# Kernel tuning notes

Hardware: AMD Instinct MI355X
Metric: run time of the kernel (lower is better)

The kernel has to match this reference:

```python
import jax, jax.numpy as jnp
import numpy as np

N, K, C = 10000, 64, 128


def setup_inputs() -> dict:
    key = jax.random.key(0)
    ks = jax.random.split(key, 6)
    return {
        "real": jax.random.normal(ks[0], (N, C), dtype=jnp.float32),
        "imag": jax.random.normal(ks[1], (N, C), dtype=jnp.float32),
        "Qreal": jax.random.normal(ks[2], (N, K), dtype=jnp.float32) / np.sqrt(N),
        "Qimag": jax.random.normal(ks[3], (N, K), dtype=jnp.float32) / np.sqrt(N),
        "Ritz": jax.random.uniform(ks[4], (K,), dtype=jnp.float32),
        "weight": jax.random.normal(ks[5], (C, C), dtype=jnp.float32) * np.sqrt(2.0 / (C + C)),  # xavier-ish scale
        "long_diff": 5,
    }


def reference(real, imag, Qreal, Qimag, Ritz, weight, long_diff):
    # TT = Ritz ** long_diff ; spectral filters L = Q diag(TT) Q^H split into real/imag
    TT = jnp.power(Ritz, long_diff)  # [K]
    QrT = Qreal * TT  # [N,K] columns scaled by TT (== Qreal @ diag(TT))
    QiT = Qimag * TT
    L_real = QrT @ Qreal.T + QiT @ Qimag.T  # [N,N]
    L_imag = QiT @ Qreal.T - QrT @ Qimag.T  # [N,N]
    # complex spmm + shared dense weight: (L @ X_complex) @ W
    res_real = (L_real @ real - L_imag @ imag) @ weight  # [N,C]
    res_imag = (L_imag @ real + L_real @ imag) @ weight  # [N,C]
    # complex ReLU: mask by sign of real part
    mask = (res_real >= 0).astype(res_real.dtype)
    return real + mask * res_real, imag + mask * res_imag
```

## Files before the change

kernel.cpp:

```cpp
#include <hip/hip_runtime.h>

#define NN 10000
#define KK 64
#define CC 128
#define OUTOFF (NN * CC)

__device__ __forceinline__ float4 f4fma(float s, float4 v, float4 a) {
    a.x += s * v.x; a.y += s * v.y; a.z += s * v.z; a.w += s * v.w;
    return a;
}

__global__ __launch_bounds__(512) void kA(const float* __restrict__ re,
                                          const float* __restrict__ im,
                                          const float* __restrict__ Qr,
                                          const float* __restrict__ Qi,
                                          float* __restrict__ part, int nA)
{
    __shared__ float4 sQr[16][16];
    __shared__ float4 sQi[16][16];
    __shared__ float4 sRe[16][32];
    __shared__ float4 sIm[16][32];

    const int t  = threadIdx.x;
    const int kt = t & 15;
    const int ct = t >> 4;

    float aU[4][4], aV[4][4];
#pragma unroll
    for (int a = 0; a < 4; ++a)
#pragma unroll
        for (int b = 0; b < 4; ++b) { aU[a][b] = 0.f; aV[a][b] = 0.f; }

    for (int cb = blockIdx.x; cb < 625; cb += nA) {
        const int n0 = cb * 16;
        for (int i = t; i < 1536; i += 512) {
            if (i < 256) {
                int row = i >> 4, q = i & 15;
                sQr[row][q] = ((const float4*)(Qr + (size_t)(n0 + row) * KK))[q];
            } else if (i < 512) {
                int j = i - 256, row = j >> 4, q = j & 15;
                sQi[row][q] = ((const float4*)(Qi + (size_t)(n0 + row) * KK))[q];
            } else if (i < 1024) {
                int j = i - 512, row = j >> 5, q = j & 31;
                sRe[row][q] = ((const float4*)(re + (size_t)(n0 + row) * CC))[q];
            } else {
                int j = i - 1024, row = j >> 5, q = j & 31;
                sIm[row][q] = ((const float4*)(im + (size_t)(n0 + row) * CC))[q];
            }
        }
        __syncthreads();
#pragma unroll 4
        for (int r = 0; r < 16; ++r) {
            float4 q_r = sQr[r][kt];
            float4 q_i = sQi[r][kt];
            float4 x_r = sRe[r][ct];
            float4 x_i = sIm[r][ct];
            float qr[4] = {q_r.x, q_r.y, q_r.z, q_r.w};
            float qi[4] = {q_i.x, q_i.y, q_i.z, q_i.w};
            float xr[4] = {x_r.x, x_r.y, x_r.z, x_r.w};
            float xi[4] = {x_i.x, x_i.y, x_i.z, x_i.w};
#pragma unroll
            for (int a = 0; a < 4; ++a)
#pragma unroll
                for (int b = 0; b < 4; ++b) {
                    aU[a][b] += qr[a] * xr[b] + qi[a] * xi[b];
                    aV[a][b] += qi[a] * xr[b] - qr[a] * xi[b];
                }
        }
        __syncthreads();
    }
    float* base = part + (size_t)blockIdx.x * 16384;
    const int k0 = kt * 4, c0 = ct * 4;
#pragma unroll
    for (int a = 0; a < 4; ++a) {
        *(float4*)(base + (k0 + a) * CC + c0)        = make_float4(aU[a][0], aU[a][1], aU[a][2], aU[a][3]);
        *(float4*)(base + 8192 + (k0 + a) * CC + c0) = make_float4(aV[a][0], aV[a][1], aV[a][2], aV[a][3]);
    }
}

__global__ __launch_bounds__(256) void kR(const float* __restrict__ part,
                                          float* __restrict__ UV, int nA)
{
    __shared__ float red[256];
    const int t  = threadIdx.x;
    const int e0 = blockIdx.x * 32;
    const int ei = t & 31, sl = t >> 5;
    float s = 0.f;
    for (int b = sl; b < nA; b += 8)
        s += part[(size_t)b * 16384 + e0 + ei];
    red[t] = s;
    __syncthreads();
    if (t < 32) {
        float tot = 0.f;
#pragma unroll
        for (int q = 0; q < 8; ++q) tot += red[q * 32 + t];
        UV[e0 + t] = tot;
    }
}

__global__ __launch_bounds__(256) void kB(const float* __restrict__ UV,
                                          const float* __restrict__ Ritz,
                                          const int* __restrict__ ldp,
                                          const float* __restrict__ W,
                                          float* __restrict__ UVW)
{
    __shared__ float rowU[128], rowV[128];
    const int k = blockIdx.x, t = threadIdx.x;
    if (t < 128) rowU[t] = UV[k * 128 + t];
    else         rowV[t - 128] = UV[8192 + k * 128 + (t - 128)];
    __syncthreads();
    const int m = t >> 7, c = t & 127;
    const float* row = m ? rowV : rowU;
    float acc = 0.f;
#pragma unroll 8
    for (int cp = 0; cp < 128; ++cp)
        acc += row[cp] * W[cp * 128 + c];
    const int ld = *ldp;
    const float rz = Ritz[k];
    float tt = 1.f;
    for (int i = 0; i < ld; ++i) tt *= rz;
    UVW[m * 8192 + k * 128 + c] = tt * acc;
}

__global__ __launch_bounds__(256) void kC(const float* __restrict__ re,
                                          const float* __restrict__ im,
                                          const float* __restrict__ Qr,
                                          const float* __restrict__ Qi,
                                          const float* __restrict__ UVW,
                                          float* __restrict__ out)
{
    __shared__ float4 sUW[64][32];
    __shared__ float4 sVW[64][32];
    const int t = threadIdx.x;
    {
        const float4* g = (const float4*)UVW;
        float4* s0 = &sUW[0][0];
        float4* s1 = &sVW[0][0];
        for (int i = t; i < 2048; i += 256) s0[i] = g[i];
        for (int i = t; i < 2048; i += 256) s1[i] = g[2048 + i];
    }
    __syncthreads();
    const int ct = t & 15;
    const int rp = t >> 4;

    for (int cb = blockIdx.x; cb < 313; cb += 256) {
        const int na = cb * 32 + rp * 2;
        if (na >= NN) continue;
        const int nb = na + 1;
        const float4* qra = (const float4*)(Qr + (size_t)na * KK);
        const float4* qia = (const float4*)(Qi + (size_t)na * KK);
        const float4* qrb = (const float4*)(Qr + (size_t)nb * KK);
        const float4* qib = (const float4*)(Qi + (size_t)nb * KK);

        float4 z = make_float4(0.f, 0.f, 0.f, 0.f);
        float4 aR0a = z, aR1a = z, aI0a = z, aI1a = z;
        float4 aR0b = z, aR1b = z, aI0b = z, aI1b = z;

#pragma unroll 4
        for (int k4 = 0; k4 < 16; ++k4) {
            float4 QRa = qra[k4], QIa = qia[k4];
            float4 QRb = qrb[k4], QIb = qib[k4];
            float ar[4] = {QRa.x, QRa.y, QRa.z, QRa.w};
            float ai[4] = {QIa.x, QIa.y, QIa.z, QIa.w};
            float br[4] = {QRb.x, QRb.y, QRb.z, QRb.w};
            float bi[4] = {QIb.x, QIb.y, QIb.z, QIb.w};
#pragma unroll
            for (int j = 0; j < 4; ++j) {
                const int k = k4 * 4 + j;
                float4 uw0 = sUW[k][ct], uw1 = sUW[k][16 + ct];
                float4 vw0 = sVW[k][ct], vw1 = sVW[k][16 + ct];
                aR0a = f4fma(ar[j], uw0, aR0a); aR0a = f4fma(ai[j], vw0, aR0a);
                aR1a = f4fma(ar[j], uw1, aR1a); aR1a = f4fma(ai[j], vw1, aR1a);
                aI0a = f4fma(ai[j], uw0, aI0a); aI0a = f4fma(-ar[j], vw0, aI0a);
                aI1a = f4fma(ai[j], uw1, aI1a); aI1a = f4fma(-ar[j], vw1, aI1a);
                aR0b = f4fma(br[j], uw0, aR0b); aR0b = f4fma(bi[j], vw0, aR0b);
                aR1b = f4fma(br[j], uw1, aR1b); aR1b = f4fma(bi[j], vw1, aR1b);
                aI0b = f4fma(bi[j], uw0, aI0b); aI0b = f4fma(-br[j], vw0, aI0b);
                aI1b = f4fma(bi[j], uw1, aI1b); aI1b = f4fma(-br[j], vw1, aI1b);
            }
        }
        const int c0 = ct * 4;
#pragma unroll
        for (int half = 0; half < 2; ++half) {
            const int cc = c0 + half * 64;
            const float4 aRa = half ? aR1a : aR0a;
            const float4 aIa = half ? aI1a : aI0a;
            const float4 aRb = half ? aR1b : aR0b;
            const float4 aIb = half ? aI1b : aI0b;

            float4 rin = *(const float4*)(re + (size_t)na * CC + cc);
            float4 iin = *(const float4*)(im + (size_t)na * CC + cc);
            float4 orr, oii;
            orr.x = rin.x + (aRa.x >= 0.f ? aRa.x : 0.f); oii.x = iin.x + (aRa.x >= 0.f ? aIa.x : 0.f);
            orr.y = rin.y + (aRa.y >= 0.f ? aRa.y : 0.f); oii.y = iin.y + (aRa.y >= 0.f ? aIa.y : 0.f);
            orr.z = rin.z + (aRa.z >= 0.f ? aRa.z : 0.f); oii.z = iin.z + (aRa.z >= 0.f ? aIa.z : 0.f);
            orr.w = rin.w + (aRa.w >= 0.f ? aRa.w : 0.f); oii.w = iin.w + (aRa.w >= 0.f ? aIa.w : 0.f);
            *(float4*)(out + (size_t)na * CC + cc)          = orr;
            *(float4*)(out + OUTOFF + (size_t)na * CC + cc) = oii;

            rin = *(const float4*)(re + (size_t)nb * CC + cc);
            iin = *(const float4*)(im + (size_t)nb * CC + cc);
            orr.x = rin.x + (aRb.x >= 0.f ? aRb.x : 0.f); oii.x = iin.x + (aRb.x >= 0.f ? aIb.x : 0.f);
            orr.y = rin.y + (aRb.y >= 0.f ? aRb.y : 0.f); oii.y = iin.y + (aRb.y >= 0.f ? aIb.y : 0.f);
            orr.z = rin.z + (aRb.z >= 0.f ? aRb.z : 0.f); oii.z = iin.z + (aRb.z >= 0.f ? aIb.z : 0.f);
            orr.w = rin.w + (aRb.w >= 0.f ? aRb.w : 0.f); oii.w = iin.w + (aRb.w >= 0.f ? aIb.w : 0.f);
            *(float4*)(out + (size_t)nb * CC + cc)          = orr;
            *(float4*)(out + OUTOFF + (size_t)nb * CC + cc) = oii;
        }
    }
}

extern "C" void kernel_launch(void* const* d_in, const int* in_sizes, int n_in,
                              void* d_out, int out_size, void* d_ws, size_t ws_size,
                              hipStream_t stream) {
    const float* re   = (const float*)d_in[0];
    const float* im   = (const float*)d_in[1];
    const float* Qr   = (const float*)d_in[2];
    const float* Qi   = (const float*)d_in[3];
    const float* Ritz = (const float*)d_in[4];
    const float* W    = (const float*)d_in[5];
    const int*   ldp  = (const int*)d_in[6];
    float* out = (float*)d_out;
    float* ws  = (float*)d_ws;

    long avail = ((long)ws_size - 131072L) / 65536L;
    int nA = (int)(avail < 1 ? 1 : (avail > 256 ? 256 : avail));

    float* part = ws;
    float* UV   = ws + (size_t)nA * 16384;
    float* UVW  = UV + 16384;

    kA<<<nA, 512, 0, stream>>>(re, im, Qr, Qi, part, nA);
    kR<<<512, 256, 0, stream>>>(part, UV, nA);
    kB<<<64, 256, 0, stream>>>(UV, Ritz, ldp, W, UVW);
    kC<<<256, 256, 0, stream>>>(re, im, Qr, Qi, UVW, out);
}
```

Measured before the change: 126.7 us.

## Fuse four kernels into one cooperative kernel with grid syncs

Replaces the four separate launches (partial projection, reduction, weight multiply, output expansion) with a single cooperative kernel of 256 blocks of 512 threads, using grid.sync between phases. The first phase also prefetches the next chunk into registers while computing on the current one, and the output phase now gives each thread one row instead of two. The aim is to remove launch gaps and inter-kernel drain. In exchange it adds grid-wide barrier costs and fixes the partial count at 256 regardless of workspace size, and phase 3 runs on only 64 blocks while the rest wait.

```diff
diff --git a/kernel.cpp b/kernel.cpp
--- a/kernel.cpp
+++ b/kernel.cpp
@@ -1,211 +1,187 @@
 #include <hip/hip_runtime.h>
+#include <hip/hip_cooperative_groups.h>
+
+namespace cg = cooperative_groups;
 
 #define NN 10000
 #define KK 64
 #define CC 128
 #define OUTOFF (NN * CC)
+#define NA 256
+#define CHUNKS_A 625
+#define CHUNKS_C 313
 
 __device__ __forceinline__ float4 f4fma(float s, float4 v, float4 a) {
-    a.x += s * v.x; a.y += s * v.y; a.z += s * v.z; a.w += s * v.w;
+    a.x = fmaf(s, v.x, a.x); a.y = fmaf(s, v.y, a.y);
+    a.z = fmaf(s, v.z, a.z); a.w = fmaf(s, v.w, a.w);
     return a;
 }
 
-__global__ __launch_bounds__(512) void kA(const float* __restrict__ re,
-                                          const float* __restrict__ im,
-                                          const float* __restrict__ Qr,
-                                          const float* __restrict__ Qi,
-                                          float* __restrict__ part, int nA)
+__global__ __launch_bounds__(512, 1) void fused(
+    const float* __restrict__ re, const float* __restrict__ im,
+    const float* __restrict__ Qr, const float* __restrict__ Qi,
+    const float* __restrict__ Ritz, const int* __restrict__ ldp,
+    const float* __restrict__ W, float* __restrict__ ws,
+    float* __restrict__ out)
 {
-    __shared__ float4 sQr[16][16];
-    __shared__ float4 sQi[16][16];
-    __shared__ float4 sRe[16][32];
-    __shared__ float4 sIm[16][32];
-
-    const int t  = threadIdx.x;
-    const int kt = t & 15;
-    const int ct = t >> 4;
-
-    float aU[4][4], aV[4][4];
-#pragma unroll
-    for (int a = 0; a < 4; ++a)
-#pragma unroll
-        for (int b = 0; b < 4; ++b) { aU[a][b] = 0.f; aV[a][b] = 0.f; }
-
-    for (int cb = blockIdx.x; cb < 625; cb += nA) {
-        const int n0 = cb * 16;
-        for (int i = t; i < 1536; i += 512) {
-            if (i < 256) {
-                int row = i >> 4, q = i & 15;
-                sQr[row][q] = ((const float4*)(Qr + (size_t)(n0 + row) * KK))[q];
-            } else if (i < 512) {
-                int j = i - 256, row = j >> 4, q = j & 15;
-                sQi[row][q] = ((const float4*)(Qi + (size_t)(n0 + row) * KK))[q];
-            } else if (i < 1024) {
-                int j = i - 512, row = j >> 5, q = j & 31;
-                sRe[row][q] = ((const float4*)(re + (size_t)(n0 + row) * CC))[q];
-            } else {
-                int j = i - 1024, row = j >> 5, q = j & 31;
-                sIm[row][q] = ((const float4*)(im + (size_t)(n0 + row) * CC))[q];
-            }
-        }
-        __syncthreads();
+    __shared__ float4 smem[4096];
+    cg::grid_group grid = cg::this_grid();
+    const int t = threadIdx.x;
+    const int bid = blockIdx.x;
+
+    {
+        const int kt = t & 15;
+        const int ctA = t >> 4;
+        const int row_q = (t & 255) >> 4, q_q = t & 15;
+        const int row_x = t >> 5,          q_x = t & 31;
+        const float4* gq  = (const float4*)((t < 256) ? Qr : Qi);
+        const float4* gre = (const float4*)re;
+        const float4* gim = (const float4*)im;
+
+        float aU[4][4] = {}, aV[4][4] = {};
+
+        int cb = bid;
+        int n0 = cb * 16;
+        float4 r0 = gq [(size_t)(n0 + row_q) * 16 + q_q];
+        float4 r1 = gre[(size_t)(n0 + row_x) * 32 + q_x];
+        float4 r2 = gim[(size_t)(n0 + row_x) * 32 + q_x];
+
+        while (true) {
+            smem[t] = r0; smem[512 + t] = r1; smem[1024 + t] = r2;
+            __syncthreads();
+            const int nx = cb + NA;
+            if (nx < CHUNKS_A) {
+                const int m0 = nx * 16;
+                r0 = gq [(size_t)(m0 + row_q) * 16 + q_q];
+                r1 = gre[(size_t)(m0 + row_x) * 32 + q_x];
+                r2 = gim[(size_t)(m0 + row_x) * 32 + q_x];
+            }
 #pragma unroll 4
-        for (int r = 0; r < 16; ++r) {
-            float4 q_r = sQr[r][kt];
-            float4 q_i = sQi[r][kt];
-            float4 x_r = sRe[r][ct];
-            float4 x_i = sIm[r][ct];
-            float qr[4] = {q_r.x, q_r.y, q_r.z, q_r.w};
-            float qi[4] = {q_i.x, q_i.y, q_i.z, q_i.w};
-            float xr[4] = {x_r.x, x_r.y, x_r.z, x_r.w};
-            float xi[4] = {x_i.x, x_i.y, x_i.z, x_i.w};
-#pragma unroll
-            for (int a = 0; a < 4; ++a)
-#pragma unroll
-                for (int b = 0; b < 4; ++b) {
-                    aU[a][b] += qr[a] * xr[b] + qi[a] * xi[b];
-                    aV[a][b] += qi[a] * xr[b] - qr[a] * xi[b];
+            for (int rr = 0; rr < 16; ++rr) {
+                float4 q_r = smem[rr * 16 + kt];
+                float4 q_i = smem[256 + rr * 16 + kt];
+                float4 x_r = smem[512 + rr * 32 + ctA];
+                float4 x_i = smem[1024 + rr * 32 + ctA];
+                float qr_[4] = {q_r.x, q_r.y, q_r.z, q_r.w};
+                float qi_[4] = {q_i.x, q_i.y, q_i.z, q_i.w};
+                float xr_[4] = {x_r.x, x_r.y, x_r.z, x_r.w};
+                float xi_[4] = {x_i.x, x_i.y, x_i.z, x_i.w};
+#pragma unroll
+                for (int a = 0; a < 4; ++a)
+#pragma unroll
+                    for (int b = 0; b < 4; ++b) {
+                        aU[a][b] = fmaf(qr_[a], xr_[b], aU[a][b]);
+                        aU[a][b] = fmaf(qi_[a], xi_[b], aU[a][b]);
+                        aV[a][b] = fmaf(qi_[a], xr_[b], aV[a][b]);
+                        aV[a][b] = fmaf(-qr_[a], xi_[b], aV[a][b]);
+                    }
+            }
+            __syncthreads();
+            if (nx >= CHUNKS_A) break;
+            cb = nx;
+        }
+        float* base = ws + (size_t)bid * 16384;
+        const int k0 = kt * 4, c0 = ctA * 4;
+#pragma unroll
+        for (int a = 0; a < 4; ++a) {
+            *(float4*)(base + (k0 + a) * CC + c0)        = make_float4(aU[a][0], aU[a][1], aU[a][2], aU[a][3]);
+            *(float4*)(base + 8192 + (k0 + a) * CC + c0) = make_float4(aV[a][0], aV[a][1], aV[a][2], aV[a][3]);
+        }
+    }
+    __threadfence();
+    grid.sync();
+
+    {
+        const int ei = t & 63, sl = t >> 6;
+        float s = 0.f;
+        const float* p = ws + (size_t)sl * 16384 + bid * 64 + ei;
+        for (int b = sl; b < NA; b += 8) { s += *p; p += (size_t)8 * 16384; }
+        float* sf = (float*)smem;
+        sf[t] = s;
+        __syncthreads();
+        if (t < 64) {
+            float tot = 0.f;
+#pragma unroll
+            for (int q = 0; q < 8; ++q) tot += sf[q * 64 + t];
+            ws[(size_t)NA * 16384 + bid * 64 + t] = tot;
+        }
+        __syncthreads();
+    }
+    __threadfence();
+    grid.sync();
+
+    if (bid < KK) {
+        const float* UV = ws + (size_t)NA * 16384;
+        float* sf = (float*)smem;
+        if (t < 256) sf[t] = (t < 128) ? UV[bid * 128 + t]
+                                       : UV[8192 + bid * 128 + (t - 128)];
+        __syncthreads();
+        if (t < 256) {
+            const int m = t >> 7, c = t & 127;
+            const float* rowm = sf + m * 128;
+            float acc = 0.f;
+#pragma unroll 8
+            for (int cp = 0; cp < 128; ++cp)
+                acc = fmaf(rowm[cp], W[cp * 128 + c], acc);
+            const int ld = *ldp;
+            const float rz = Ritz[bid];
+            float tt = 1.f;
+            for (int i = 0; i < ld; ++i) tt *= rz;
+            ws[(size_t)NA * 16384 + 16384 + m * 8192 + bid * 128 + c] = tt * acc;
+        }
+        __syncthreads();
+    }
+    __threadfence();
+    grid.sync();
+
+    {
+        const float4* gUVW = (const float4*)(ws + (size_t)NA * 16384 + 16384);
+        for (int i = t; i < 4096; i += 512) smem[i] = gUVW[i];
+        __syncthreads();
+        const int ct = t & 15;
+        const int r  = t >> 4;
+
+        for (int cb = bid; cb < CHUNKS_C; cb += NA) {
+            const int na = cb * 32 + r;
+            if (na >= NN) continue;
+            const float4* qr4 = (const float4*)(Qr + (size_t)na * KK);
+            const float4* qi4 = (const float4*)(Qi + (size_t)na * KK);
+            float4 z = make_float4(0.f, 0.f, 0.f, 0.f);
+            float4 aR0 = z, aR1 = z, aI0 = z, aI1 = z;
+#pragma unroll 4
+            for (int k4 = 0; k4 < 16; ++k4) {
+                float4 QR = qr4[k4], QI = qi4[k4];
+                float ar[4] = {QR.x, QR.y, QR.z, QR.w};
+                float ai[4] = {QI.x, QI.y, QI.z, QI.w};
+#pragma unroll
+                for (int j = 0; j < 4; ++j) {
+                    const int k = k4 * 4 + j;
+                    float4 uw0 = smem[k * 32 + ct];
+                    float4 uw1 = smem[k * 32 + 16 + ct];
+                    float4 vw0 = smem[2048 + k * 32 + ct];
+                    float4 vw1 = smem[2048 + k * 32 + 16 + ct];
+                    aR0 = f4fma(ar[j], uw0, aR0); aR0 = f4fma(ai[j], vw0, aR0);
+                    aR1 = f4fma(ar[j], uw1, aR1); aR1 = f4fma(ai[j], vw1, aR1);
+                    aI0 = f4fma(ai[j], uw0, aI0); aI0 = f4fma(-ar[j], vw0, aI0);
+                    aI1 = f4fma(ai[j], uw1, aI1); aI1 = f4fma(-ar[j], vw1, aI1);
                 }
-        }
-        __syncthreads();
-    }
-    float* base = part + (size_t)blockIdx.x * 16384;
-    const int k0 = kt * 4, c0 = ct * 4;
-#pragma unroll
-    for (int a = 0; a < 4; ++a) {
-        *(float4*)(base + (k0 + a) * CC + c0)        = make_float4(aU[a][0], aU[a][1], aU[a][2], aU[a][3]);
-        *(float4*)(base + 8192 + (k0 + a) * CC + c0) = make_float4(aV[a][0], aV[a][1], aV[a][2], aV[a][3]);
-    }
-}
-
-__global__ __launch_bounds__(256) void kR(const float* __restrict__ part,
-                                          float* __restrict__ UV, int nA)
-{
-    __shared__ float red[256];
-    const int t  = threadIdx.x;
-    const int e0 = blockIdx.x * 32;
-    const int ei = t & 31, sl = t >> 5;
-    float s = 0.f;
-    for (int b = sl; b < nA; b += 8)
-        s += part[(size_t)b * 16384 + e0 + ei];
-    red[t] = s;
-    __syncthreads();
-    if (t < 32) {
-        float tot = 0.f;
-#pragma unroll
-        for (int q = 0; q < 8; ++q) tot += red[q * 32 + t];
-        UV[e0 + t] = tot;
-    }
-}
-
-__global__ __launch_bounds__(256) void kB(const float* __restrict__ UV,
-                                          const float* __restrict__ Ritz,
-                                          const int* __restrict__ ldp,
-                                          const float* __restrict__ W,
-                                          float* __restrict__ UVW)
-{
-    __shared__ float rowU[128], rowV[128];
-    const int k = blockIdx.x, t = threadIdx.x;
-    if (t < 128) rowU[t] = UV[k * 128 + t];
-    else         rowV[t - 128] = UV[8192 + k * 128 + (t - 128)];
-    __syncthreads();
-    const int m = t >> 7, c = t & 127;
-    const float* row = m ? rowV : rowU;
-    float acc = 0.f;
-#pragma unroll 8
-    for (int cp = 0; cp < 128; ++cp)
-        acc += row[cp] * W[cp * 128 + c];
-    const int ld = *ldp;
-    const float rz = Ritz[k];
-    float tt = 1.f;
-    for (int i = 0; i < ld; ++i) tt *= rz;
-    UVW[m * 8192 + k * 128 + c] = tt * acc;
-}
-
-__global__ __launch_bounds__(256) void kC(const float* __restrict__ re,
-                                          const float* __restrict__ im,
-                                          const float* __restrict__ Qr,
-                                          const float* __restrict__ Qi,
-                                          const float* __restrict__ UVW,
-                                          float* __restrict__ out)
-{
-    __shared__ float4 sUW[64][32];
-    __shared__ float4 sVW[64][32];
-    const int t = threadIdx.x;
-    {
-        const float4* g = (const float4*)UVW;
-        float4* s0 = &sUW[0][0];
-        float4* s1 = &sVW[0][0];
-        for (int i = t; i < 2048; i += 256) s0[i] = g[i];
-        for (int i = t; i < 2048; i += 256) s1[i] = g[2048 + i];
-    }
-    __syncthreads();
-    const int ct = t & 15;
-    const int rp = t >> 4;
-
-    for (int cb = blockIdx.x; cb < 313; cb += 256) {
-        const int na = cb * 32 + rp * 2;
-        if (na >= NN) continue;
-        const int nb = na + 1;
-        const float4* qra = (const float4*)(Qr + (size_t)na * KK);
-        const float4* qia = (const float4*)(Qi + (size_t)na * KK);
-        const float4* qrb = (const float4*)(Qr + (size_t)nb * KK);
-        const float4* qib = (const float4*)(Qi + (size_t)nb * KK);
-
-        float4 z = make_float4(0.f, 0.f, 0.f, 0.f);
-        float4 aR0a = z, aR1a = z, aI0a = z, aI1a = z;
-        float4 aR0b = z, aR1b = z, aI0b = z, aI1b = z;
-
-#pragma unroll 4
-        for (int k4 = 0; k4 < 16; ++k4) {
-            float4 QRa = qra[k4], QIa = qia[k4];
-            float4 QRb = qrb[k4], QIb = qib[k4];
-            float ar[4] = {QRa.x, QRa.y, QRa.z, QRa.w};
-            float ai[4] = {QIa.x, QIa.y, QIa.z, QIa.w};
-            float br[4] = {QRb.x, QRb.y, QRb.z, QRb.w};
-            float bi[4] = {QIb.x, QIb.y, QIb.z, QIb.w};
-#pragma unroll
-            for (int j = 0; j < 4; ++j) {
-                const int k = k4 * 4 + j;
-                float4 uw0 = sUW[k][ct], uw1 = sUW[k][16 + ct];
-                float4 vw0 = sVW[k][ct], vw1 = sVW[k][16 + ct];
-                aR0a = f4fma(ar[j], uw0, aR0a); aR0a = f4fma(ai[j], vw0, aR0a);
-                aR1a = f4fma(ar[j], uw1, aR1a); aR1a = f4fma(ai[j], vw1, aR1a);
-                aI0a = f4fma(ai[j], uw0, aI0a); aI0a = f4fma(-ar[j], vw0, aI0a);
-                aI1a = f4fma(ai[j], uw1, aI1a); aI1a = f4fma(-ar[j], vw1, aI1a);
-                aR0b = f4fma(br[j], uw0, aR0b); aR0b = f4fma(bi[j], vw0, aR0b);
-                aR1b = f4fma(br[j], uw1, aR1b); aR1b = f4fma(bi[j], vw1, aR1b);
-                aI0b = f4fma(bi[j], uw0, aI0b); aI0b = f4fma(-br[j], vw0, aI0b);
-                aI1b = f4fma(bi[j], uw1, aI1b); aI1b = f4fma(-br[j], vw1, aI1b);
-            }
-        }
-        const int c0 = ct * 4;
-#pragma unroll
-        for (int half = 0; half < 2; ++half) {
-            const int cc = c0 + half * 64;
-            const float4 aRa = half ? aR1a : aR0a;
-            const float4 aIa = half ? aI1a : aI0a;
-            const float4 aRb = half ? aR1b : aR0b;
-            const float4 aIb = half ? aI1b : aI0b;
-
-            float4 rin = *(const float4*)(re + (size_t)na * CC + cc);
-            float4 iin = *(const float4*)(im + (size_t)na * CC + cc);
-            float4 orr, oii;
-            orr.x = rin.x + (aRa.x >= 0.f ? aRa.x : 0.f); oii.x = iin.x + (aRa.x >= 0.f ? aIa.x : 0.f);
-            orr.y = rin.y + (aRa.y >= 0.f ? aRa.y : 0.f); oii.y = iin.y + (aRa.y >= 0.f ? aIa.y : 0.f);
-            orr.z = rin.z + (aRa.z >= 0.f ? aRa.z : 0.f); oii.z = iin.z + (aRa.z >= 0.f ? aIa.z : 0.f);
-            orr.w = rin.w + (aRa.w >= 0.f ? aRa.w : 0.f); oii.w = iin.w + (aRa.w >= 0.f ? aIa.w : 0.f);
-            *(float4*)(out + (size_t)na * CC + cc)          = orr;
-            *(float4*)(out + OUTOFF + (size_t)na * CC + cc) = oii;
-
-            rin = *(const float4*)(re + (size_t)nb * CC + cc);
-            iin = *(const float4*)(im + (size_t)nb * CC + cc);
-            orr.x = rin.x + (aRb.x >= 0.f ? aRb.x : 0.f); oii.x = iin.x + (aRb.x >= 0.f ? aIb.x : 0.f);
-            orr.y = rin.y + (aRb.y >= 0.f ? aRb.y : 0.f); oii.y = iin.y + (aRb.y >= 0.f ? aIb.y : 0.f);
-            orr.z = rin.z + (aRb.z >= 0.f ? aRb.z : 0.f); oii.z = iin.z + (aRb.z >= 0.f ? aIb.z : 0.f);
-            orr.w = rin.w + (aRb.w >= 0.f ? aRb.w : 0.f); oii.w = iin.w + (aRb.w >= 0.f ? aIb.w : 0.f);
-            *(float4*)(out + (size_t)nb * CC + cc)          = orr;
-            *(float4*)(out + OUTOFF + (size_t)nb * CC + cc) = oii;
+            }
+            const int c0 = ct * 4;
+#pragma unroll
+            for (int half = 0; half < 2; ++half) {
+                const int cc = c0 + half * 64;
+                const float4 aR = half ? aR1 : aR0;
+                const float4 aI = half ? aI1 : aI0;
+                float4 rin = *(const float4*)(re + (size_t)na * CC + cc);
+                float4 iin = *(const float4*)(im + (size_t)na * CC + cc);
+                float4 orr, oii;
+                orr.x = rin.x + (aR.x >= 0.f ? aR.x : 0.f); oii.x = iin.x + (aR.x >= 0.f ? aI.x : 0.f);
+                orr.y = rin.y + (aR.y >= 0.f ? aR.y : 0.f); oii.y = iin.y + (aR.y >= 0.f ? aI.y : 0.f);
+                orr.z = rin.z + (aR.z >= 0.f ? aR.z : 0.f); oii.z = iin.z + (aR.z >= 0.f ? aI.z : 0.f);
+                orr.w = rin.w + (aR.w >= 0.f ? aR.w : 0.f); oii.w = iin.w + (aR.w >= 0.f ? aI.w : 0.f);
+                *(float4*)(out + (size_t)na * CC + cc)          = orr;
+                *(float4*)(out + OUTOFF + (size_t)na * CC + cc) = oii;
+            }
         }
     }
 }
@@ -223,15 +199,7 @@
     float* out = (float*)d_out;
     float* ws  = (float*)d_ws;
 
-    long avail = ((long)ws_size - 131072L) / 65536L;
-    int nA = (int)(avail < 1 ? 1 : (avail > 256 ? 256 : avail));
-
-    float* part = ws;
-    float* UV   = ws + (size_t)nA * 16384;
-    float* UVW  = UV + 16384;
-
-    kA<<<nA, 512, 0, stream>>>(re, im, Qr, Qi, part, nA);
-    kR<<<512, 256, 0, stream>>>(part, UV, nA);
-    kB<<<64, 256, 0, stream>>>(UV, Ritz, ldp, W, UVW);
-    kC<<<256, 256, 0, stream>>>(re, im, Qr, Qi, UVW, out);
+    void* args[] = { (void*)&re, (void*)&im, (void*)&Qr, (void*)&Qi,
+                     (void*)&Ritz, (void*)&ldp, (void*)&W, (void*)&ws, (void*)&out };
+    hipLaunchCooperativeKernel((void*)fused, dim3(NA), dim3(512), args, 0, stream);
 }
```

Result: slower. 336.8 us (+165.7%).

## Fuse partial reduction with weight GEMM, prefetch kA tiles, one-shot kC grid

Applied to the files above, without the earlier changes.

Merges the partial-sum reduction kernel and the Ritz-scaled weight multiply into a single kernel, which removes one launch and the round trip through UV. kA now loads the next chunk into registers while the current one is being computed, so global load latency overlaps the FMA loop. kC launches one block per 32-row chunk instead of grid-striding, and its shared arrays are split so the two column halves use separate buffers. The workspace-dependent block count is replaced by a fixed 256, which assumes the workspace is large enough.

```diff
diff --git a/kernel.cpp b/kernel.cpp
--- a/kernel.cpp
+++ b/kernel.cpp
@@ -4,73 +4,77 @@
 #define KK 64
 #define CC 128
 #define OUTOFF (NN * CC)
+#define NA 256
+#define CHUNKS_A 625
+#define CHUNKS_C 313
 
 __device__ __forceinline__ float4 f4fma(float s, float4 v, float4 a) {
-    a.x += s * v.x; a.y += s * v.y; a.z += s * v.z; a.w += s * v.w;
+    a.x = fmaf(s, v.x, a.x); a.y = fmaf(s, v.y, a.y);
+    a.z = fmaf(s, v.z, a.z); a.w = fmaf(s, v.w, a.w);
     return a;
 }
+
 
 __global__ __launch_bounds__(512) void kA(const float* __restrict__ re,
                                           const float* __restrict__ im,
                                           const float* __restrict__ Qr,
                                           const float* __restrict__ Qi,
-                                          float* __restrict__ part, int nA)
+                                          float* __restrict__ part)
 {
-    __shared__ float4 sQr[16][16];
-    __shared__ float4 sQi[16][16];
-    __shared__ float4 sRe[16][32];
-    __shared__ float4 sIm[16][32];
-
-    const int t  = threadIdx.x;
+    __shared__ float4 smem[1536];
+    const int t = threadIdx.x;
+    const int bid = blockIdx.x;
     const int kt = t & 15;
-    const int ct = t >> 4;
-
-    float aU[4][4], aV[4][4];
-#pragma unroll
-    for (int a = 0; a < 4; ++a)
-#pragma unroll
-        for (int b = 0; b < 4; ++b) { aU[a][b] = 0.f; aV[a][b] = 0.f; }
-
-    for (int cb = blockIdx.x; cb < 625; cb += nA) {
-        const int n0 = cb * 16;
-        for (int i = t; i < 1536; i += 512) {
-            if (i < 256) {
-                int row = i >> 4, q = i & 15;
-                sQr[row][q] = ((const float4*)(Qr + (size_t)(n0 + row) * KK))[q];
-            } else if (i < 512) {
-                int j = i - 256, row = j >> 4, q = j & 15;
-                sQi[row][q] = ((const float4*)(Qi + (size_t)(n0 + row) * KK))[q];
-            } else if (i < 1024) {
-                int j = i - 512, row = j >> 5, q = j & 31;
-                sRe[row][q] = ((const float4*)(re + (size_t)(n0 + row) * CC))[q];
-            } else {
-                int j = i - 1024, row = j >> 5, q = j & 31;
-                sIm[row][q] = ((const float4*)(im + (size_t)(n0 + row) * CC))[q];
-            }
-        }
+    const int ctA = t >> 4;
+    const int row_q = (t & 255) >> 4, q_q = t & 15;
+    const int row_x = t >> 5,          q_x = t & 31;
+    const float4* gq  = (const float4*)((t < 256) ? Qr : Qi);
+    const float4* gre = (const float4*)re;
+    const float4* gim = (const float4*)im;
+
+    float aU[4][4] = {}, aV[4][4] = {};
+
+    int cb = bid;
+    float4 r0 = gq [(size_t)(cb * 16 + row_q) * 16 + q_q];
+    float4 r1 = gre[(size_t)(cb * 16 + row_x) * 32 + q_x];
+    float4 r2 = gim[(size_t)(cb * 16 + row_x) * 32 + q_x];
+
+    while (true) {
+        smem[t] = r0; smem[512 + t] = r1; smem[1024 + t] = r2;
         __syncthreads();
+        const int nx = cb + NA;
+        if (nx < CHUNKS_A) {
+            const int m0 = nx * 16;
+            r0 = gq [(size_t)(m0 + row_q) * 16 + q_q];
+            r1 = gre[(size_t)(m0 + row_x) * 32 + q_x];
+            r2 = gim[(size_t)(m0 + row_x) * 32 + q_x];
+        }
 #pragma unroll 4
-        for (int r = 0; r < 16; ++r) {
-            float4 q_r = sQr[r][kt];
-            float4 q_i = sQi[r][kt];
-            float4 x_r = sRe[r][ct];
-            float4 x_i = sIm[r][ct];
-            float qr[4] = {q_r.x, q_r.y, q_r.z, q_r.w};
-            float qi[4] = {q_i.x, q_i.y, q_i.z, q_i.w};
-            float xr[4] = {x_r.x, x_r.y, x_r.z, x_r.w};
-            float xi[4] = {x_i.x, x_i.y, x_i.z, x_i.w};
+        for (int rr = 0; rr < 16; ++rr) {
+            float4 q_r = smem[rr * 16 + kt];
+            float4 q_i = smem[256 + rr * 16 + kt];
+            float4 x_r = smem[512 + rr * 32 + ctA];
+            float4 x_i = smem[1024 + rr * 32 + ctA];
+            float qr_[4] = {q_r.x, q_r.y, q_r.z, q_r.w};
+            float qi_[4] = {q_i.x, q_i.y, q_i.z, q_i.w};
+            float xr_[4] = {x_r.x, x_r.y, x_r.z, x_r.w};
+            float xi_[4] = {x_i.x, x_i.y, x_i.z, x_i.w};
 #pragma unroll
             for (int a = 0; a < 4; ++a)
 #pragma unroll
                 for (int b = 0; b < 4; ++b) {
-                    aU[a][b] += qr[a] * xr[b] + qi[a] * xi[b];
-                    aV[a][b] += qi[a] * xr[b] - qr[a] * xi[b];
+                    aU[a][b] = fmaf(qr_[a], xr_[b], aU[a][b]);
+                    aU[a][b] = fmaf(qi_[a], xi_[b], aU[a][b]);
+                    aV[a][b] = fmaf(qi_[a], xr_[b], aV[a][b]);
+                    aV[a][b] = fmaf(-qr_[a], xi_[b], aV[a][b]);
                 }
         }
         __syncthreads();
-    }
-    float* base = part + (size_t)blockIdx.x * 16384;
-    const int k0 = kt * 4, c0 = ct * 4;
+        if (nx >= CHUNKS_A) break;
+        cb = nx;
+    }
+    float* base = part + (size_t)bid * 16384;
+    const int k0 = kt * 4, c0 = ctA * 4;
 #pragma unroll
     for (int a = 0; a < 4; ++a) {
         *(float4*)(base + (k0 + a) * CC + c0)        = make_float4(aU[a][0], aU[a][1], aU[a][2], aU[a][3]);
@@ -78,48 +82,43 @@
     }
 }
 
-__global__ __launch_bounds__(256) void kR(const float* __restrict__ part,
-                                          float* __restrict__ UV, int nA)
+__global__ __launch_bounds__(512) void kRB(const float* __restrict__ part,
+                                           const float* __restrict__ Ritz,
+                                           const int* __restrict__ ldp,
+                                           const float* __restrict__ W,
+                                           float* __restrict__ UVW)
 {
-    __shared__ float red[256];
-    const int t  = threadIdx.x;
-    const int e0 = blockIdx.x * 32;
-    const int ei = t & 31, sl = t >> 5;
-    float s = 0.f;
-    for (int b = sl; b < nA; b += 8)
-        s += part[(size_t)b * 16384 + e0 + ei];
-    red[t] = s;
+    __shared__ float red[512];
+    __shared__ float rowS[128];
+    const int t = threadIdx.x;
+    const int m = blockIdx.x >> 6, k = blockIdx.x & 63;
+    const int c = t & 127, bl = t >> 7;
+
+    const float* p = part + (size_t)bl * 16384 + m * 8192 + k * 128 + c;
+    float s0 = 0.f, s1 = 0.f, s2 = 0.f, s3 = 0.f;
+#pragma unroll 4
+    for (int jj = 0; jj < 16; ++jj) {
+        s0 += p[0];
+        s1 += p[4  * 16384];
+        s2 += p[8  * 16384];
+        s3 += p[12 * 16384];
+        p += 16 * 16384;
+    }
+    red[t] = s0 + s1 + s2 + s3;
     __syncthreads();
-    if (t < 32) {
-        float tot = 0.f;
-#pragma unroll
-        for (int q = 0; q < 8; ++q) tot += red[q * 32 + t];
-        UV[e0 + t] = tot;
-    }
-}
-
-__global__ __launch_bounds__(256) void kB(const float* __restrict__ UV,
-                                          const float* __restrict__ Ritz,
-                                          const int* __restrict__ ldp,
-                                          const float* __restrict__ W,
-                                          float* __restrict__ UVW)
-{
-    __shared__ float rowU[128], rowV[128];
-    const int k = blockIdx.x, t = threadIdx.x;
-    if (t < 128) rowU[t] = UV[k * 128 + t];
-    else         rowV[t - 128] = UV[8192 + k * 128 + (t - 128)];
+    if (t < 128) rowS[t] = red[t] + red[t + 128] + red[t + 256] + red[t + 384];
     __syncthreads();
-    const int m = t >> 7, c = t & 127;
-    const float* row = m ? rowV : rowU;
-    float acc = 0.f;
+    if (t < 128) {
+        float acc = 0.f;
 #pragma unroll 8
-    for (int cp = 0; cp < 128; ++cp)
-        acc += row[cp] * W[cp * 128 + c];
-    const int ld = *ldp;
-    const float rz = Ritz[k];
-    float tt = 1.f;
-    for (int i = 0; i < ld; ++i) tt *= rz;
-    UVW[m * 8192 + k * 128 + c] = tt * acc;
+        for (int cp = 0; cp < 128; ++cp)
+            acc = fmaf(rowS[cp], W[cp * 128 + t], acc);
+        const int ld = *ldp;
+        const float rz = Ritz[k];
+        float tt = 1.f;
+        for (int i = 0; i < ld; ++i) tt *= rz;
+        UVW[m * 8192 + k * 128 + t] = tt * acc;
+    }
 }
 
 __global__ __launch_bounds__(256) void kC(const float* __restrict__ re,
@@ -129,84 +128,90 @@
                                           const float* __restrict__ UVW,
                                           float* __restrict__ out)
 {
-    __shared__ float4 sUW[64][32];
-    __shared__ float4 sVW[64][32];
+    __shared__ float4 sUW[64][16];
+    __shared__ float4 sVW[64][16];
+    __shared__ float4 sUW1[64][16];
+    __shared__ float4 sVW1[64][16];
     const int t = threadIdx.x;
     {
         const float4* g = (const float4*)UVW;
-        float4* s0 = &sUW[0][0];
-        float4* s1 = &sVW[0][0];
-        for (int i = t; i < 2048; i += 256) s0[i] = g[i];
-        for (int i = t; i < 2048; i += 256) s1[i] = g[2048 + i];
+        for (int i = t; i < 2048; i += 256) {
+            int k = i >> 5, q = i & 31;
+            float4 v = g[i];
+            if (q < 16) sUW[k][q] = v; else sUW1[k][q - 16] = v;
+        }
+        for (int i = t; i < 2048; i += 256) {
+            int k = i >> 5, q = i & 31;
+            float4 v = g[2048 + i];
+            if (q < 16) sVW[k][q] = v; else sVW1[k][q - 16] = v;
+        }
     }
     __syncthreads();
     const int ct = t & 15;
     const int rp = t >> 4;
 
-    for (int cb = blockIdx.x; cb < 313; cb += 256) {
-        const int na = cb * 32 + rp * 2;
-        if (na >= NN) continue;
-        const int nb = na + 1;
-        const float4* qra = (const float4*)(Qr + (size_t)na * KK);
-        const float4* qia = (const float4*)(Qi + (size_t)na * KK);
-        const float4* qrb = (const float4*)(Qr + (size_t)nb * KK);
-        const float4* qib = (const float4*)(Qi + (size_t)nb * KK);
-
-        float4 z = make_float4(0.f, 0.f, 0.f, 0.f);
-        float4 aR0a = z, aR1a = z, aI0a = z, aI1a = z;
-        float4 aR0b = z, aR1b = z, aI0b = z, aI1b = z;
+    const int na = blockIdx.x * 32 + rp * 2;
+    if (na >= NN) return;
+    const int nb = na + 1;
+    const float4* qra = (const float4*)(Qr + (size_t)na * KK);
+    const float4* qia = (const float4*)(Qi + (size_t)na * KK);
+    const float4* qrb = (const float4*)(Qr + (size_t)nb * KK);
+    const float4* qib = (const float4*)(Qi + (size_t)nb * KK);
+
+    float4 z = make_float4(0.f, 0.f, 0.f, 0.f);
+    float4 aR0a = z, aR1a = z, aI0a = z, aI1a = z;
+    float4 aR0b = z, aR1b = z, aI0b = z, aI1b = z;
 
 #pragma unroll 4
-        for (int k4 = 0; k4 < 16; ++k4) {
-            float4 QRa = qra[k4], QIa = qia[k4];
-            float4 QRb = qrb[k4], QIb = qib[k4];
-            float ar[4] = {QRa.x, QRa.y, QRa.z, QRa.w};
-            float ai[4] = {QIa.x, QIa.y, QIa.z, QIa.w};
-            float br[4] = {QRb.x, QRb.y, QRb.z, QRb.w};
-            float bi[4] = {QIb.x, QIb.y, QIb.z, QIb.w};
-#pragma unroll
-            for (int j = 0; j < 4; ++j) {
-                const int k = k4 * 4 + j;
-                float4 uw0 = sUW[k][ct], uw1 = sUW[k][16 + ct];
-                float4 vw0 = sVW[k][ct], vw1 = sVW[k][16 + ct];
-                aR0a = f4fma(ar[j], uw0, aR0a); aR0a = f4fma(ai[j], vw0, aR0a);
-                aR1a = f4fma(ar[j], uw1, aR1a); aR1a = f4fma(ai[j], vw1, aR1a);
-                aI0a = f4fma(ai[j], uw0, aI0a); aI0a = f4fma(-ar[j], vw0, aI0a);
-                aI1a = f4fma(ai[j], uw1, aI1a); aI1a = f4fma(-ar[j], vw1, aI1a);
-                aR0b = f4fma(br[j], uw0, aR0b); aR0b = f4fma(bi[j], vw0, aR0b);
-                aR1b = f4fma(br[j], uw1, aR1b); aR1b = f4fma(bi[j], vw1, aR1b);
-                aI0b = f4fma(bi[j], uw0, aI0b); aI0b = f4fma(-br[j], vw0, aI0b);
-                aI1b = f4fma(bi[j], uw1, aI1b); aI1b = f4fma(-br[j], vw1, aI1b);
-            }
-        }
-        const int c0 = ct * 4;
-#pragma unroll
-        for (int half = 0; half < 2; ++half) {
-            const int cc = c0 + half * 64;
-            const float4 aRa = half ? aR1a : aR0a;
-            const float4 aIa = half ? aI1a : aI0a;
-            const float4 aRb = half ? aR1b : aR0b;
-            const float4 aIb = half ? aI1b : aI0b;
-
-            float4 rin = *(const float4*)(re + (size_t)na * CC + cc);
-            float4 iin = *(const float4*)(im + (size_t)na * CC + cc);
-            float4 orr, oii;
-            orr.x = rin.x + (aRa.x >= 0.f ? aRa.x : 0.f); oii.x = iin.x + (aRa.x >= 0.f ? aIa.x : 0.f);
-            orr.y = rin.y + (aRa.y >= 0.f ? aRa.y : 0.f); oii.y = iin.y + (aRa.y >= 0.f ? aIa.y : 0.f);
-            orr.z = rin.z + (aRa.z >= 0.f ? aRa.z : 0.f); oii.z = iin.z + (aRa.z >= 0.f ? aIa.z : 0.f);
-            orr.w = rin.w + (aRa.w >= 0.f ? aRa.w : 0.f); oii.w = iin.w + (aRa.w >= 0.f ? aIa.w : 0.f);
-            *(float4*)(out + (size_t)na * CC + cc)          = orr;
-            *(float4*)(out + OUTOFF + (size_t)na * CC + cc) = oii;
-
-            rin = *(const float4*)(re + (size_t)nb * CC + cc);
-            iin = *(const float4*)(im + (size_t)nb * CC + cc);
-            orr.x = rin.x + (aRb.x >= 0.f ? aRb.x : 0.f); oii.x = iin.x + (aRb.x >= 0.f ? aIb.x : 0.f);
-            orr.y = rin.y + (aRb.y >= 0.f ? aRb.y : 0.f); oii.y = iin.y + (aRb.y >= 0.f ? aIb.y : 0.f);
-            orr.z = rin.z + (aRb.z >= 0.f ? aRb.z : 0.f); oii.z = iin.z + (aRb.z >= 0.f ? aIb.z : 0.f);
-            orr.w = rin.w + (aRb.w >= 0.f ? aRb.w : 0.f); oii.w = iin.w + (aRb.w >= 0.f ? aIb.w : 0.f);
-            *(float4*)(out + (size_t)nb * CC + cc)          = orr;
-            *(float4*)(out + OUTOFF + (size_t)nb * CC + cc) = oii;
-        }
+    for (int k4 = 0; k4 < 16; ++k4) {
+        float4 QRa = qra[k4], QIa = qia[k4];
+        float4 QRb = qrb[k4], QIb = qib[k4];
+        float ar[4] = {QRa.x, QRa.y, QRa.z, QRa.w};
+        float ai[4] = {QIa.x, QIa.y, QIa.z, QIa.w};
+        float br[4] = {QRb.x, QRb.y, QRb.z, QRb.w};
+        float bi[4] = {QIb.x, QIb.y, QIb.z, QIb.w};
+#pragma unroll
+        for (int j = 0; j < 4; ++j) {
+            const int k = k4 * 4 + j;
+            float4 uw0 = sUW[k][ct],  uw1 = sUW1[k][ct];
+            float4 vw0 = sVW[k][ct],  vw1 = sVW1[k][ct];
+            aR0a = f4fma(ar[j], uw0, aR0a); aR0a = f4fma(ai[j], vw0, aR0a);
+            aR1a = f4fma(ar[j], uw1, aR1a); aR1a = f4fma(ai[j], vw1, aR1a);
+            aI0a = f4fma(ai[j], uw0, aI0a); aI0a = f4fma(-ar[j], vw0, aI0a);
+            aI1a = f4fma(ai[j], uw1, aI1a); aI1a = f4fma(-ar[j], vw1, aI1a);
+            aR0b = f4fma(br[j], uw0, aR0b); aR0b = f4fma(bi[j], vw0, aR0b);
+            aR1b = f4fma(br[j], uw1, aR1b); aR1b = f4fma(bi[j], vw1, aR1b);
+            aI0b = f4fma(bi[j], uw0, aI0b); aI0b = f4fma(-br[j], vw0, aI0b);
+            aI1b = f4fma(bi[j], uw1, aI1b); aI1b = f4fma(-br[j], vw1, aI1b);
+        }
+    }
+    const int c0 = ct * 4;
+#pragma unroll
+    for (int half = 0; half < 2; ++half) {
+        const int cc = c0 + half * 64;
+        const float4 aRa = half ? aR1a : aR0a;
+        const float4 aIa = half ? aI1a : aI0a;
+        const float4 aRb = half ? aR1b : aR0b;
+        const float4 aIb = half ? aI1b : aI0b;
+
+        float4 rin = *(const float4*)(re + (size_t)na * CC + cc);
+        float4 iin = *(const float4*)(im + (size_t)na * CC + cc);
+        float4 orr, oii;
+        orr.x = rin.x + (aRa.x >= 0.f ? aRa.x : 0.f); oii.x = iin.x + (aRa.x >= 0.f ? aIa.x : 0.f);
+        orr.y = rin.y + (aRa.y >= 0.f ? aRa.y : 0.f); oii.y = iin.y + (aRa.y >= 0.f ? aIa.y : 0.f);
+        orr.z = rin.z + (aRa.z >= 0.f ? aRa.z : 0.f); oii.z = iin.z + (aRa.z >= 0.f ? aIa.z : 0.f);
+        orr.w = rin.w + (aRa.w >= 0.f ? aRa.w : 0.f); oii.w = iin.w + (aRa.w >= 0.f ? aIa.w : 0.f);
+        *(float4*)(out + (size_t)na * CC + cc)          = orr;
+        *(float4*)(out + OUTOFF + (size_t)na * CC + cc) = oii;
+
+        rin = *(const float4*)(re + (size_t)nb * CC + cc);
+        iin = *(const float4*)(im + (size_t)nb * CC + cc);
+        orr.x = rin.x + (aRb.x >= 0.f ? aRb.x : 0.f); oii.x = iin.x + (aRb.x >= 0.f ? aIb.x : 0.f);
+        orr.y = rin.y + (aRb.y >= 0.f ? aRb.y : 0.f); oii.y = iin.y + (aRb.y >= 0.f ? aIb.y : 0.f);
+        orr.z = rin.z + (aRb.z >= 0.f ? aRb.z : 0.f); oii.z = iin.z + (aRb.z >= 0.f ? aIb.z : 0.f);
+        orr.w = rin.w + (aRb.w >= 0.f ? aRb.w : 0.f); oii.w = iin.w + (aRb.w >= 0.f ? aIb.w : 0.f);
+        *(float4*)(out + (size_t)nb * CC + cc)          = orr;
+        *(float4*)(out + OUTOFF + (size_t)nb * CC + cc) = oii;
     }
 }
 
@@ -223,15 +228,10 @@
     float* out = (float*)d_out;
     float* ws  = (float*)d_ws;
 
-    long avail = ((long)ws_size - 131072L) / 65536L;
-    int nA = (int)(avail < 1 ? 1 : (avail > 256 ? 256 : avail));
-
     float* part = ws;
-    float* UV   = ws + (size_t)nA * 16384;
-    float* UVW  = UV + 16384;
-
-    kA<<<nA, 512, 0, stream>>>(re, im, Qr, Qi, part, nA);
-    kR<<<512, 256, 0, stream>>>(part, UV, nA);
-    kB<<<64, 256, 0, stream>>>(UV, Ritz, ldp, W, UVW);
-    kC<<<256, 256, 0, stream>>>(re, im, Qr, Qi, UVW, out);
-}
+    float* UVW  = ws + (size_t)NA * 16384;
+
+    kA <<<NA,       512, 0, stream>>>(re, im, Qr, Qi, part);
+    kRB<<<128,      512, 0, stream>>>(part, Ritz, ldp, W, UVW);
+    kC <<<CHUNKS_C, 256, 0, stream>>>(re, im, Qr, Qi, UVW, out);
+}
```

Result: faster. 121.7 us (-3.9%).
